# Optimization experiments

Measured on AMD Instinct MI355X. Metric: run time of the kernel, lower is better.

Reference implementation:

```python
import jax, jax.numpy as jnp
import numpy as np

T, V, E, K, D, H, BERT = 4, 4096, 4096, 32, 8, 16, 768
CAT = H + BERT  # 784, second LSTM input size


def setup_inputs() -> dict:
    key = jax.random.key(0)
    ks = jax.random.split(key, 24)
    n = lambda k, s: jax.random.normal(k, s, dtype=jnp.float32) * 0.02
    return dict(
        prices=jax.random.normal(ks[0], (T, V, 1), dtype=jnp.float32),
        node_embs=jax.random.normal(ks[1], (T, E, BERT), dtype=jnp.float32),
        he_members=jax.random.randint(ks[2], (T, E, K), 0, V),
        vert_edges=jax.random.randint(ks[3], (T, V, D), 0, E),
        Wih_p=n(ks[4], (4 * H, 1)), Whh_p=n(ks[5], (4 * H, H)),
        bih_p=n(ks[6], (4 * H,)), bhh_p=n(ks[7], (4 * H,)),
        Wih_m=n(ks[8], (4 * H, CAT)), Whh_m=n(ks[9], (4 * H, H)),
        bih_m=n(ks[10], (4 * H,)), bhh_m=n(ks[11], (4 * H,)),
        vc_trans_w=n(ks[12], (K, K, H)), vc_trans_b=n(ks[13], (K, K)),
        vc_conv_w=n(ks[14], (K,)), vc_conv_b=n(ks[15], (1,)),
        ec_w1=n(ks[16], (CAT // 4, CAT)), ec_b1=n(ks[17], (CAT // 4,)),
        ec_w2=n(ks[18], (1, CAT // 4)), ec_b2=n(ks[19], (1,)),
        attn_in=n(ks[20], (H, H)), attn_out=n(ks[21], (H, 2 * H)),
        fc_w=n(ks[22], (2, H)), fc_b=n(ks[23], (2,)),
    )


def _lstm(x, Wih, Whh, bih, bhh):
    # x: (T, B, in) -> hidden states (T, B, H); PyTorch gate order i,f,g,o
    h0 = jnp.zeros((x.shape[1], Whh.shape[1]), x.dtype)
    b = bih + bhh

    def step(carry, xt):
        h, c = carry
        g = xt @ Wih.T + h @ Whh.T + b
        i, f, gg, o = jnp.split(g, 4, axis=-1)
        c = jax.nn.sigmoid(f) * c + jax.nn.sigmoid(i) * jnp.tanh(gg)
        h = jax.nn.sigmoid(o) * jnp.tanh(c)
        return (h, c), h

    _, hs = jax.lax.scan(step, (h0, h0), x)
    return hs


def reference(prices, node_embs, he_members, vert_edges,
              Wih_p, Whh_p, bih_p, bhh_p,
              Wih_m, Whh_m, bih_m, bhh_m,
              vc_trans_w, vc_trans_b, vc_conv_w, vc_conv_b,
              ec_w1, ec_b1, ec_w2, ec_b2,
              attn_in, attn_out, fc_w, fc_b):
    # price LSTM over lookback window: (T, V, 1) -> (T, V, H)
    new_prices = _lstm(prices, Wih_p, Whh_p, bih_p, bhh_p)

    # --- VertexConv (DHGNN): gather member price embeddings per hyperedge ---
    # reg[t,e,k] = new_prices[t, he_members[t,e,k]]  -> (T, E, K, H)
    reg = jax.vmap(lambda p, idx: p[idx])(new_prices, he_members)
    # grouped Conv1d(k, k*k, dim_in, groups=k): row i of multiplier depends on feat i
    mult = jnp.einsum('tekd,kjd->tekj', reg, vc_trans_w) + vc_trans_b
    mult = jax.nn.softmax(mult, axis=-1)                     # (T,E,K,K)
    trans = jnp.einsum('tekj,tejd->tekd', mult, reg)         # (T,E,K,H)
    he_emb = jnp.einsum('tekd,k->ted', trans, vc_conv_w) + vc_conv_b  # (T,E,H)

    # concat hyperedge emb with article embedding -> (T, E, 784)
    he_cat = jnp.concatenate([he_emb, node_embs], axis=-1)

    # --- EdgeConv: per-vertex attention over its D adjacent hyperedges ---
    ft = jax.vmap(lambda h, idx: h[idx])(he_cat, vert_edges)  # (T,V,D,CAT)
    s = jax.nn.relu(ft @ ec_w1.T + ec_b1) @ ec_w2.T + ec_b2   # (T,V,D,1)
    w = jax.nn.softmax(s, axis=2)
    hg = jnp.sum(w * ft, axis=2)                              # (T,V,CAT) == scatter into hg_tensor

    # second LSTM + residual with price embeddings
    lstm_out = _lstm(hg, Wih_m, Whh_m, bih_m, bhh_m)          # (T,V,H)
    la = lstm_out + new_prices

    # torchnlp 'general' Attention: query = last step, context = all steps
    q = la[-1] @ attn_in.T                                    # (V,H)
    ctx = jnp.transpose(la, (1, 0, 2))                        # (V,T,H)
    aw = jax.nn.softmax(jnp.einsum('vd,vtd->vt', q, ctx), axis=-1)
    mix = jnp.einsum('vt,vtd->vd', aw, ctx)
    attn = jnp.tanh(jnp.concatenate([mix, q], axis=-1) @ attn_out.T)  # (V,H)

    # final classifier (dropout identity in eval)
    return attn @ fc_w.T + fc_b                               # (V,2)
```

## Files before the change

### kernel.cpp

```cpp
#include <hip/hip_runtime.h>
#include <hip/hip_bf16.h>
#include <math.h>

#define TT 4
#define VV 4096
#define EE 4096
#define KK 32
#define DD 8
#define HH 16
#define BERTD 768
#define CATD 784
#define NH 196
#define NTOT 260
#define KPB 800
#define NPB 288
#define LDB 808

typedef __bf16 bf16x8 __attribute__((ext_vector_type(8)));
typedef float  f32x4  __attribute__((ext_vector_type(4)));

__device__ __forceinline__ float sigmoidf_(float x){ return 1.0f/(1.0f+expf(-x)); }
__device__ __forceinline__ unsigned short f2bf(float f){
  __bf16 h = (__bf16)f;
  return __builtin_bit_cast(unsigned short, h);
}
__device__ __forceinline__ float bf2f(unsigned short u){
  unsigned int x = ((unsigned int)u) << 16;
  return __builtin_bit_cast(float, x);
}
__device__ __forceinline__ bf16x8 cvt_bf8(float4 a, float4 b){
  bf16x8 r;
  r[0]=(__bf16)a.x; r[1]=(__bf16)a.y; r[2]=(__bf16)a.z; r[3]=(__bf16)a.w;
  r[4]=(__bf16)b.x; r[5]=(__bf16)b.y; r[6]=(__bf16)b.z; r[7]=(__bf16)b.w;
  return r;
}

__global__ __launch_bounds__(256) void kP(
    const float* __restrict__ prices,
    const float* __restrict__ Wih, const float* __restrict__ Whh,
    const float* __restrict__ bih, const float* __restrict__ bhh,
    float* __restrict__ np_out,
    const float* __restrict__ w1, const float* __restrict__ wm,
    unsigned short* __restrict__ Bbf,
    const float* __restrict__ tw, unsigned short* __restrict__ twbf,
    float* __restrict__ esc){
  int b = blockIdx.x;
  int tid = threadIdx.x;
  if (b < 256){
    int lane = tid & 15;
    int v    = (b*256 + tid) >> 4;
    float W[4][16], wih[4], bb[4];
#pragma unroll
    for (int gi=0; gi<4; ++gi){
      int j = gi*16 + lane;
      const float4* wr = reinterpret_cast<const float4*>(&Whh[j*16]);
      float4 w0=wr[0], w1v=wr[1], w2v=wr[2], w3v=wr[3];
      W[gi][0]=w0.x; W[gi][1]=w0.y; W[gi][2]=w0.z; W[gi][3]=w0.w;
      W[gi][4]=w1v.x; W[gi][5]=w1v.y; W[gi][6]=w1v.z; W[gi][7]=w1v.w;
      W[gi][8]=w2v.x; W[gi][9]=w2v.y; W[gi][10]=w2v.z; W[gi][11]=w2v.w;
      W[gi][12]=w3v.x; W[gi][13]=w3v.y; W[gi][14]=w3v.z; W[gi][15]=w3v.w;
      wih[gi] = Wih[j];
      bb[gi]  = bih[j] + bhh[j];
    }
    float h = 0.f, c = 0.f;
    for (int t=0; t<TT; ++t){
      float x = prices[t*VV + v];
      float a0 = fmaf(x, wih[0], bb[0]);
      float a1 = fmaf(x, wih[1], bb[1]);
      float a2 = fmaf(x, wih[2], bb[2]);
      float a3 = fmaf(x, wih[3], bb[3]);
#pragma unroll
      for (int d=0; d<16; ++d){
        float hb = __shfl(h, d, 16);
        a0 = fmaf(hb, W[0][d], a0);
        a1 = fmaf(hb, W[1][d], a1);
        a2 = fmaf(hb, W[2][d], a2);
        a3 = fmaf(hb, W[3][d], a3);
      }
      float ig = sigmoidf_(a0);
      float fg = sigmoidf_(a1);
      float gg = tanhf(a2);
      float og = sigmoidf_(a3);
      c = fmaf(fg, c, ig*gg);
      h = og * tanhf(c);
      np_out[(size_t)(t*VV+v)*16 + lane] = h;
    }
  } else if (b < 544){
    int n = b - 256;
    const float* src = nullptr;
    if (n < NH)        src = &w1[(size_t)n*CATD];
    else if (n < NTOT) src = &wm[(size_t)(n-NH)*CATD];
    for (int kx = tid; kx < KPB; kx += 256){
      float v = (src != nullptr && kx < CATD) ? src[kx] : 0.f;
      Bbf[(size_t)n*KPB + kx] = f2bf(v);
    }
  } else if (b < 546){
    int base = (b - 544) * 512;
#pragma unroll
    for (int rr = 0; rr < 2; ++rr){
      int r = base + tid*2 + rr;
      const float* s = &tw[(size_t)r*16];
#pragma unroll
      for (int d = 0; d < 16; ++d) twbf[(size_t)r*16 + d] = f2bf(s[d]);
    }
  } else {
    int idx = ((b - 546)*256 + tid)*4;
    float4 z = make_float4(0.f,0.f,0.f,0.f);
    *reinterpret_cast<float4*>(&esc[idx]) = z;
  }
}

__global__ __launch_bounds__(256) void k2_fused(
    const float* __restrict__ np, const int* __restrict__ mem,
    const unsigned short* __restrict__ twbf, const float* __restrict__ tb,
    const float* __restrict__ cw, const float* __restrict__ cb,
    float* __restrict__ he_emb){
  __shared__ unsigned short s_reg[32*16*16];
  __shared__ float s_wsumP[4][16][32];
  __shared__ int   s_mem[512];
  int tid = threadIdx.x;
  int te0 = blockIdx.x * 16;
  for (int i = tid; i < 512; i += 256) s_mem[i] = mem[(size_t)te0*32 + i];
  __syncthreads();
  for (int p = tid; p < 512; p += 256){
    int gte = p & 15, gk = p >> 4;
    int t   = (te0 + gte) >> 12;
    int vid = s_mem[gte*32 + gk];
    const float4* src = reinterpret_cast<const float4*>(&np[((size_t)(t*VV) + vid)*16]);
    float4 f0 = src[0], f1 = src[1], f2 = src[2], f3 = src[3];
    uint4 u0, u1;
    u0.x = (unsigned)f2bf(f0.x) | ((unsigned)f2bf(f0.y) << 16);
    u0.y = (unsigned)f2bf(f0.z) | ((unsigned)f2bf(f0.w) << 16);
    u0.z = (unsigned)f2bf(f1.x) | ((unsigned)f2bf(f1.y) << 16);
    u0.w = (unsigned)f2bf(f1.z) | ((unsigned)f2bf(f1.w) << 16);
    u1.x = (unsigned)f2bf(f2.x) | ((unsigned)f2bf(f2.y) << 16);
    u1.y = (unsigned)f2bf(f2.z) | ((unsigned)f2bf(f2.w) << 16);
    u1.z = (unsigned)f2bf(f3.x) | ((unsigned)f2bf(f3.y) << 16);
    u1.w = (unsigned)f2bf(f3.z) | ((unsigned)f2bf(f3.w) << 16);
    uint4* dst = reinterpret_cast<uint4*>(&s_reg[(gk*16 + gte)*16]);
    dst[0] = u0; dst[1] = u1;
  }
  __syncthreads();
  int l = tid & 63;
  int w = tid >> 6;
  int lj = l & 15;
  int lg = l >> 4;
  float w0acc[4] = {0.f,0.f,0.f,0.f};
  float w1acc[4] = {0.f,0.f,0.f,0.f};
#pragma unroll
  for (int kk = 0; kk < 8; ++kk){
    int k = w*8 + kk;
    bf16x8 af = 0, b0 = 0, b1v = 0;
    if (l < 32){
      af  = *reinterpret_cast<const bf16x8*>(&s_reg[(k*16 + lj)*16 + lg*8]);
      b0  = *reinterpret_cast<const bf16x8*>(&twbf[((size_t)k*32 + lj)*16 + lg*8]);
      b1v = *reinterpret_cast<const bf16x8*>(&twbf[((size_t)k*32 + 16 + lj)*16 + lg*8]);
    }
    float tb0 = tb[k*32 + lj];
    float tb1 = tb[k*32 + 16 + lj];
    f32x4 c0 = {tb0, tb0, tb0, tb0};
    f32x4 c1 = {tb1, tb1, tb1, tb1};
    f32x4 s0 = __builtin_amdgcn_mfma_f32_16x16x32_bf16(af, b0,  c0, 0, 0, 0);
    f32x4 s1 = __builtin_amdgcn_mfma_f32_16x16x32_bf16(af, b1v, c1, 0, 0, 0);
    float cwk = cw[k];
#pragma unroll
    for (int i = 0; i < 4; ++i){
      float v0 = s0[i], v1 = s1[i];
      float m = fmaxf(v0, v1);
#pragma unroll
      for (int off = 1; off < 16; off <<= 1) m = fmaxf(m, __shfl_xor(m, off, 16));
      float e0 = expf(v0 - m), e1 = expf(v1 - m);
      float sm = e0 + e1;
#pragma unroll
      for (int off = 1; off < 16; off <<= 1) sm += __shfl_xor(sm, off, 16);
      float f = cwk / sm;
      w0acc[i] = fmaf(e0, f, w0acc[i]);
      w1acc[i] = fmaf(e1, f, w1acc[i]);
    }
  }
#pragma unroll
  for (int i = 0; i < 4; ++i){
    int ter = lg*4 + i;
    s_wsumP[w][ter][lj]      = w0acc[i];
    s_wsumP[w][ter][16 + lj] = w1acc[i];
  }
  __syncthreads();
  int te = tid >> 4, d = tid & 15;
  float he = cb[0];
#pragma unroll
  for (int j = 0; j < 32; ++j){
    float ws = s_wsumP[0][te][j] + s_wsumP[1][te][j]
             + s_wsumP[2][te][j] + s_wsumP[3][te][j];
    he = fmaf(ws, bf2f(s_reg[(j*16 + te)*16 + d]), he);
  }
  he_emb[((size_t)(te0 + te))*16 + d] = he;
}

__global__ __launch_bounds__(256) void k3_gemm_mfma(
    const float* __restrict__ he_emb, const float* __restrict__ node,
    const unsigned short* __restrict__ Bbf, const float* __restrict__ b1,
    const float* __restrict__ w2, float* __restrict__ esc,
    float* __restrict__ C_pe){
  __shared__ unsigned short Bs[48*LDB];
  int tid = threadIdx.x;
  int nc = blockIdx.x;
  int mb = blockIdx.y;
  for (int i = tid; i < 4800; i += 256){
    int r = i / 100, c = i - r*100;
    *reinterpret_cast<uint4*>(&Bs[r*LDB + c*8]) =
      *reinterpret_cast<const uint4*>(&Bbf[(size_t)(nc*48 + r)*KPB + c*8]);
  }
  __syncthreads();
  int l = tid & 63, w = tid >> 6;
  int lr = l & 15, ls = l >> 4;
  int m0 = mb*128 + w*32;
  int row0 = m0 + lr, row1 = m0 + 16 + lr;
  const unsigned short* bbase = &Bs[lr*LDB + ls*8];
  f32x4 acc[2][3] = {};
#pragma unroll
  for (int s = 0; s < 25; ++s){
    bf16x8 af0 = 0, af1 = 0;
    if (s == 0){
      if (ls < 2){
        const float4* p0 = reinterpret_cast<const float4*>(&he_emb[(size_t)row0*16 + ls*8]);
        const float4* p1 = reinterpret_cast<const float4*>(&he_emb[(size_t)row1*16 + ls*8]);
        af0 = cvt_bf8(p0[0], p0[1]);
        af1 = cvt_bf8(p1[0], p1[1]);
      } else {
        const float4* p0 = reinterpret_cast<const float4*>(&node[(size_t)row0*BERTD + ls*8 - 16]);
        const float4* p1 = reinterpret_cast<const float4*>(&node[(size_t)row1*BERTD + ls*8 - 16]);
        af0 = cvt_bf8(p0[0], p0[1]);
        af1 = cvt_bf8(p1[0], p1[1]);
      }
    } else if (!(s == 24 && ls >= 2)){
      int ko = s*32 + ls*8 - 16;
      const float4* p0 = reinterpret_cast<const float4*>(&node[(size_t)row0*BERTD + ko]);
      const float4* p1 = reinterpret_cast<const float4*>(&node[(size_t)row1*BERTD + ko]);
      af0 = cvt_bf8(p0[0], p0[1]);
      af1 = cvt_bf8(p1[0], p1[1]);
    }
#pragma unroll
    for (int j = 0; j < 3; ++j){
      bf16x8 bfv = *reinterpret_cast<const bf16x8*>(&bbase[j*16*LDB + s*32]);
      acc[0][j] = __builtin_amdgcn_mfma_f32_16x16x32_bf16(af0, bfv, acc[0][j], 0, 0, 0);
      acc[1][j] = __builtin_amdgcn_mfma_f32_16x16x32_bf16(af1, bfv, acc[1][j], 0, 0, 0);
    }
  }
  float p[2][4] = {{0.f,0.f,0.f,0.f},{0.f,0.f,0.f,0.f}};
#pragma unroll
  for (int j = 0; j < 3; ++j){
    int n = nc*48 + j*16 + lr;
    bool hid = (n < NH);
    float b1n = hid ? b1[n] : 0.f;
    float w2n = hid ? w2[n] : 0.f;
#pragma unroll
    for (int i = 0; i < 2; ++i){
#pragma unroll
      for (int q = 0; q < 4; ++q){
        float v = acc[i][j][q];
        if (hid){
          p[i][q] += fmaxf(v + b1n, 0.f) * w2n;
        } else if (n < NTOT){
          int m = m0 + i*16 + ls*4 + q;
          C_pe[(size_t)m*64 + (n - NH)] = v;
        }
      }
    }
  }
  if (nc*48 < NH){
#pragma unroll
    for (int i = 0; i < 2; ++i){
#pragma unroll
      for (int q = 0; q < 4; ++q){
        float v = p[i][q];
#pragma unroll
        for (int off = 1; off < 16; off <<= 1) v += __shfl_xor(v, off, 16);
        if (lr == 0){
          int m = m0 + i*16 + ls*4 + q;
          atomicAdd(&esc[m], v);
        }
      }
    }
  }
}

__global__ __launch_bounds__(256) void k456(
    const int* __restrict__ ve, const float* __restrict__ esc,
    const float* __restrict__ C_pe, const float* __restrict__ np,
    const float* __restrict__ Whh, const float* __restrict__ bih,
    const float* __restrict__ bhh,
    const float* __restrict__ ain, const float* __restrict__ aout,
    const float* __restrict__ fcw, const float* __restrict__ fcb,
    float* __restrict__ out){
  __shared__ float s_ain[16*17];
  __shared__ float s_aout[16*33];
  __shared__ float s_fc[32];
  __shared__ float s_fcb[2];
  int tid = threadIdx.x;
  { int j = tid >> 4, d = tid & 15; s_ain[j*17+d] = ain[tid]; }
  for (int i = tid; i < 512; i += 256){ int j = i >> 5, d = i & 31; s_aout[j*33+d] = aout[i]; }
  if (tid < 32) s_fc[tid] = fcw[tid];
  if (tid < 2)  s_fcb[tid] = fcb[tid];
  int lane = tid & 15;
  int v = (blockIdx.x*256 + tid) >> 4;
  float W[4][16], b[4];
#pragma unroll
  for (int gi=0; gi<4; ++gi){
    int j = gi*16 + lane;
    const float4* wr = reinterpret_cast<const float4*>(&Whh[j*16]);
    float4 w0=wr[0], w1=wr[1], w2=wr[2], w3=wr[3];
    W[gi][0]=w0.x; W[gi][1]=w0.y; W[gi][2]=w0.z; W[gi][3]=w0.w;
    W[gi][4]=w1.x; W[gi][5]=w1.y; W[gi][6]=w1.z; W[gi][7]=w1.w;
    W[gi][8]=w2.x; W[gi][9]=w2.y; W[gi][10]=w2.z; W[gi][11]=w2.w;
    W[gi][12]=w3.x; W[gi][13]=w3.y; W[gi][14]=w3.z; W[gi][15]=w3.w;
    b[gi] = bih[j] + bhh[j];
  }
  __syncthreads();
  float h = 0.f, c = 0.f;
  float la0, la1, la2, la3;
#pragma unroll
  for (int t=0; t<TT; ++t){
    const int* vp = &ve[((size_t)(t*VV) + v)*8];
    int e[8]; float wv[8];
    float mx = -1e30f;
#pragma unroll
    for (int d = 0; d < 8; ++d){
      e[d] = vp[d];
      wv[d] = esc[(t << 12) + e[d]];
      mx = fmaxf(mx, wv[d]);
    }
    float s = 0.f;
#pragma unroll
    for (int d = 0; d < 8; ++d){ wv[d] = expf(wv[d]-mx); s += wv[d]; }
    float inv = 1.f/s;
#pragma unroll
    for (int d = 0; d < 8; ++d) wv[d] *= inv;
    float g0 = b[0], g1 = b[1], g2 = b[2], g3 = b[3];
#pragma unroll
    for (int d = 0; d < 8; ++d){
      const float* cp = &C_pe[(size_t)((t << 12) + e[d])*64];
      g0 = fmaf(wv[d], cp[lane],      g0);
      g1 = fmaf(wv[d], cp[16 + lane], g1);
      g2 = fmaf(wv[d], cp[32 + lane], g2);
      g3 = fmaf(wv[d], cp[48 + lane], g3);
    }
#pragma unroll
    for (int d=0; d<16; ++d){
      float hb = __shfl(h, d, 16);
      g0 = fmaf(hb, W[0][d], g0);
      g1 = fmaf(hb, W[1][d], g1);
      g2 = fmaf(hb, W[2][d], g2);
      g3 = fmaf(hb, W[3][d], g3);
    }
    float ig = sigmoidf_(g0);
    float fg = sigmoidf_(g1);
    float gg = tanhf(g2);
    float og = sigmoidf_(g3);
    c = fmaf(fg, c, ig*gg);
    h = og * tanhf(c);
    float la = h + np[(size_t)(t*VV+v)*16 + lane];
    if (t == 0) la0 = la; else if (t == 1) la1 = la;
    else if (t == 2) la2 = la; else la3 = la;
  }
  float q = 0.f;
#pragma unroll
  for (int d=0; d<16; ++d){
    float bb = __shfl(la3, d, 16);
    q = fmaf(bb, s_ain[lane*17+d], q);
  }
  float aw0 = q*la0, aw1 = q*la1, aw2 = q*la2, aw3 = q*la3;
#pragma unroll
  for (int off=1; off<16; off<<=1){
    aw0 += __shfl_xor(aw0, off, 16);
    aw1 += __shfl_xor(aw1, off, 16);
    aw2 += __shfl_xor(aw2, off, 16);
    aw3 += __shfl_xor(aw3, off, 16);
  }
  float mx = fmaxf(fmaxf(aw0,aw1), fmaxf(aw2,aw3));
  aw0 = expf(aw0-mx); aw1 = expf(aw1-mx); aw2 = expf(aw2-mx); aw3 = expf(aw3-mx);
  float inv = 1.f/(aw0+aw1+aw2+aw3);
  float mix = (aw0*la0 + aw1*la1 + aw2*la2 + aw3*la3) * inv;
  float a = 0.f;
#pragma unroll
  for (int d=0; d<16; ++d){
    float m  = __shfl(mix, d, 16);
    float qq = __shfl(q,  d, 16);
    a = fmaf(m,  s_aout[lane*33+d],    a);
    a = fmaf(qq, s_aout[lane*33+16+d], a);
  }
  float at = tanhf(a);
  float p0 = at * s_fc[lane];
  float p1 = at * s_fc[16+lane];
#pragma unroll
  for (int off=1; off<16; off<<=1){
    p0 += __shfl_xor(p0, off, 16);
    p1 += __shfl_xor(p1, off, 16);
  }
  if (lane == 0){
    out[(size_t)v*2 + 0] = p0 + s_fcb[0];
    out[(size_t)v*2 + 1] = p1 + s_fcb[1];
  }
}

extern "C" void kernel_launch(void* const* d_in, const int* in_sizes, int n_in,
                              void* d_out, int out_size, void* d_ws, size_t ws_size,
                              hipStream_t stream){
  const float* prices = (const float*)d_in[0];
  const float* node   = (const float*)d_in[1];
  const int*   mem    = (const int*)d_in[2];
  const int*   ve     = (const int*)d_in[3];
  const float* Wih_p  = (const float*)d_in[4];
  const float* Whh_p  = (const float*)d_in[5];
  const float* bih_p  = (const float*)d_in[6];
  const float* bhh_p  = (const float*)d_in[7];
  const float* Wih_m  = (const float*)d_in[8];
  const float* Whh_m  = (const float*)d_in[9];
  const float* bih_m  = (const float*)d_in[10];
  const float* bhh_m  = (const float*)d_in[11];
  const float* tw     = (const float*)d_in[12];
  const float* tb     = (const float*)d_in[13];
  const float* cw     = (const float*)d_in[14];
  const float* cb     = (const float*)d_in[15];
  const float* w1     = (const float*)d_in[16];
  const float* b1     = (const float*)d_in[17];
  const float* w2     = (const float*)d_in[18];
  const float* ain    = (const float*)d_in[20];
  const float* aout   = (const float*)d_in[21];
  const float* fcw    = (const float*)d_in[22];
  const float* fcb    = (const float*)d_in[23];

  float* np_buf = (float*)d_ws;
  float* he_emb = np_buf + (size_t)TT*VV*HH;
  float* esc    = he_emb + (size_t)TT*EE*HH;
  float* C_pe   = esc    + (size_t)TT*EE;
  unsigned short* Bbf  = (unsigned short*)(C_pe + (size_t)TT*EE*64);
  unsigned short* twbf = Bbf + (size_t)NPB*KPB;

  kP<<<562, 256, 0, stream>>>(prices, Wih_p, Whh_p, bih_p, bhh_p, np_buf,
                              w1, Wih_m, Bbf, tw, twbf, esc);
  k2_fused<<<(TT*EE)/16, 256, 0, stream>>>(np_buf, mem, twbf, tb, cw, cb, he_emb);
  k3_gemm_mfma<<<dim3(6, 128), 256, 0, stream>>>(he_emb, node, Bbf, b1, w2, esc, C_pe);
  k456<<<(VV*16)/256, 256, 0, stream>>>(ve, esc, C_pe, np_buf, Whh_m, bih_m, bhh_m,
                                        ain, aout, fcw, fcb, (float*)d_out);
}
```

Before: 232.7 us.

## Pre-convert node embeddings to a padded bf16 A matrix and regroup GEMM blocks

Adds extra kP blocks that convert node_embs to bf16 in a padded row-major A buffer, and k2 now writes he_emb as bf16 straight into the first 16 columns of that buffer. The GEMM then loads A tiles with plain 16-byte bf16 loads instead of fp32 loads with per-element conversion and branching. It also linearises the GEMM grid so that six N-chunks of eight M-blocks are scheduled together, which should improve L2 reuse of A rows. The cost is an extra full pass that reads the fp32 embeddings and writes a bf16 copy before the GEMM.

```diff
diff --git a/kernel.cpp b/kernel.cpp
--- a/kernel.cpp
+++ b/kernel.cpp
@@ -28,11 +28,13 @@
   unsigned int x = ((unsigned int)u) << 16;
   return __builtin_bit_cast(float, x);
 }
-__device__ __forceinline__ bf16x8 cvt_bf8(float4 a, float4 b){
-  bf16x8 r;
-  r[0]=(__bf16)a.x; r[1]=(__bf16)a.y; r[2]=(__bf16)a.z; r[3]=(__bf16)a.w;
-  r[4]=(__bf16)b.x; r[5]=(__bf16)b.y; r[6]=(__bf16)b.z; r[7]=(__bf16)b.w;
-  return r;
+__device__ __forceinline__ uint4 pack8(float4 a, float4 b){
+  uint4 u;
+  u.x = (unsigned)f2bf(a.x) | ((unsigned)f2bf(a.y) << 16);
+  u.y = (unsigned)f2bf(a.z) | ((unsigned)f2bf(a.w) << 16);
+  u.z = (unsigned)f2bf(b.x) | ((unsigned)f2bf(b.y) << 16);
+  u.w = (unsigned)f2bf(b.z) | ((unsigned)f2bf(b.w) << 16);
+  return u;
 }
 
 __global__ __launch_bounds__(256) void kP(
@@ -43,7 +45,8 @@
     const float* __restrict__ w1, const float* __restrict__ wm,
     unsigned short* __restrict__ Bbf,
     const float* __restrict__ tw, unsigned short* __restrict__ twbf,
-    float* __restrict__ esc){
+    float* __restrict__ esc,
+    const float* __restrict__ node, unsigned short* __restrict__ Abf){
   int b = blockIdx.x;
   int tid = threadIdx.x;
   if (b < 256){
@@ -103,10 +106,27 @@
 #pragma unroll
       for (int d = 0; d < 16; ++d) twbf[(size_t)r*16 + d] = f2bf(s[d]);
     }
-  } else {
+  } else if (b < 562){
     int idx = ((b - 546)*256 + tid)*4;
     float4 z = make_float4(0.f,0.f,0.f,0.f);
     *reinterpret_cast<float4*>(&esc[idx]) = z;
+  } else {
+    int row = (b - 562)*16 + (tid >> 4);
+    int c0  = (tid & 15) * 48;
+    const float* src = &node[(size_t)row*BERTD + c0];
+    unsigned short* dst = &Abf[(size_t)row*KPB + 16 + c0];
+#pragma unroll
+    for (int cc = 0; cc < 6; ++cc){
+      float4 f0 = *reinterpret_cast<const float4*>(&src[cc*8]);
+      float4 f1 = *reinterpret_cast<const float4*>(&src[cc*8+4]);
+      *reinterpret_cast<uint4*>(&dst[cc*8]) = pack8(f0, f1);
+    }
+    if ((tid & 15) == 15){
+      uint4 z = {0,0,0,0};
+      unsigned short* zp = &Abf[(size_t)row*KPB + 784];
+      *reinterpret_cast<uint4*>(&zp[0]) = z;
+      *reinterpret_cast<uint4*>(&zp[8]) = z;
+    }
   }
 }
 
@@ -114,7 +134,7 @@
     const float* __restrict__ np, const int* __restrict__ mem,
     const unsigned short* __restrict__ twbf, const float* __restrict__ tb,
     const float* __restrict__ cw, const float* __restrict__ cb,
-    float* __restrict__ he_emb){
+    unsigned short* __restrict__ Abf){
   __shared__ unsigned short s_reg[32*16*16];
   __shared__ float s_wsumP[4][16][32];
   __shared__ int   s_mem[512];
@@ -128,17 +148,9 @@
     int vid = s_mem[gte*32 + gk];
     const float4* src = reinterpret_cast<const float4*>(&np[((size_t)(t*VV) + vid)*16]);
     float4 f0 = src[0], f1 = src[1], f2 = src[2], f3 = src[3];
-    uint4 u0, u1;
-    u0.x = (unsigned)f2bf(f0.x) | ((unsigned)f2bf(f0.y) << 16);
-    u0.y = (unsigned)f2bf(f0.z) | ((unsigned)f2bf(f0.w) << 16);
-    u0.z = (unsigned)f2bf(f1.x) | ((unsigned)f2bf(f1.y) << 16);
-    u0.w = (unsigned)f2bf(f1.z) | ((unsigned)f2bf(f1.w) << 16);
-    u1.x = (unsigned)f2bf(f2.x) | ((unsigned)f2bf(f2.y) << 16);
-    u1.y = (unsigned)f2bf(f2.z) | ((unsigned)f2bf(f2.w) << 16);
-    u1.z = (unsigned)f2bf(f3.x) | ((unsigned)f2bf(f3.y) << 16);
-    u1.w = (unsigned)f2bf(f3.z) | ((unsigned)f2bf(f3.w) << 16);
     uint4* dst = reinterpret_cast<uint4*>(&s_reg[(gk*16 + gte)*16]);
-    dst[0] = u0; dst[1] = u1;
+    dst[0] = pack8(f0, f1);
+    dst[1] = pack8(f2, f3);
   }
   __syncthreads();
   int l = tid & 63;
@@ -193,18 +205,22 @@
              + s_wsumP[2][te][j] + s_wsumP[3][te][j];
     he = fmaf(ws, bf2f(s_reg[(j*16 + te)*16 + d]), he);
   }
-  he_emb[((size_t)(te0 + te))*16 + d] = he;
+  Abf[((size_t)(te0 + te))*KPB + d] = f2bf(he);
 }
 
 __global__ __launch_bounds__(256) void k3_gemm_mfma(
-    const float* __restrict__ he_emb, const float* __restrict__ node,
+    const unsigned short* __restrict__ Abf,
     const unsigned short* __restrict__ Bbf, const float* __restrict__ b1,
     const float* __restrict__ w2, float* __restrict__ esc,
     float* __restrict__ C_pe){
   __shared__ unsigned short Bs[48*LDB];
   int tid = threadIdx.x;
-  int nc = blockIdx.x;
-  int mb = blockIdx.y;
+  int bid = blockIdx.x;
+  int group = bid / 48;
+  int within = bid - group*48;
+  int nc  = within >> 3;
+  int mbr = within & 7;
+  int mb  = group*8 + mbr;
   for (int i = tid; i < 4800; i += 256){
     int r = i / 100, c = i - r*100;
     *reinterpret_cast<uint4*>(&Bs[r*LDB + c*8]) =
@@ -214,31 +230,14 @@
   int l = tid & 63, w = tid >> 6;
   int lr = l & 15, ls = l >> 4;
   int m0 = mb*128 + w*32;
-  int row0 = m0 + lr, row1 = m0 + 16 + lr;
+  const unsigned short* a0p = &Abf[(size_t)(m0 + lr)*KPB];
+  const unsigned short* a1p = a0p + (size_t)16*KPB;
   const unsigned short* bbase = &Bs[lr*LDB + ls*8];
   f32x4 acc[2][3] = {};
 #pragma unroll
   for (int s = 0; s < 25; ++s){
-    bf16x8 af0 = 0, af1 = 0;
-    if (s == 0){
-      if (ls < 2){
-        const float4* p0 = reinterpret_cast<const float4*>(&he_emb[(size_t)row0*16 + ls*8]);
-        const float4* p1 = reinterpret_cast<const float4*>(&he_emb[(size_t)row1*16 + ls*8]);
-        af0 = cvt_bf8(p0[0], p0[1]);
-        af1 = cvt_bf8(p1[0], p1[1]);
-      } else {
-        const float4* p0 = reinterpret_cast<const float4*>(&node[(size_t)row0*BERTD + ls*8 - 16]);
-        const float4* p1 = reinterpret_cast<const float4*>(&node[(size_t)row1*BERTD + ls*8 - 16]);
-        af0 = cvt_bf8(p0[0], p0[1]);
-        af1 = cvt_bf8(p1[0], p1[1]);
-      }
-    } else if (!(s == 24 && ls >= 2)){
-      int ko = s*32 + ls*8 - 16;
-      const float4* p0 = reinterpret_cast<const float4*>(&node[(size_t)row0*BERTD + ko]);
-      const float4* p1 = reinterpret_cast<const float4*>(&node[(size_t)row1*BERTD + ko]);
-      af0 = cvt_bf8(p0[0], p0[1]);
-      af1 = cvt_bf8(p1[0], p1[1]);
-    }
+    bf16x8 af0 = *reinterpret_cast<const bf16x8*>(&a0p[s*32 + ls*8]);
+    bf16x8 af1 = *reinterpret_cast<const bf16x8*>(&a1p[s*32 + ls*8]);
 #pragma unroll
     for (int j = 0; j < 3; ++j){
       bf16x8 bfv = *reinterpret_cast<const bf16x8*>(&bbase[j*16*LDB + s*32]);
@@ -430,16 +429,16 @@
   const float* fcb    = (const float*)d_in[23];
 
   float* np_buf = (float*)d_ws;
-  float* he_emb = np_buf + (size_t)TT*VV*HH;
-  float* esc    = he_emb + (size_t)TT*EE*HH;
+  float* esc    = np_buf + (size_t)TT*VV*HH;
   float* C_pe   = esc    + (size_t)TT*EE;
   unsigned short* Bbf  = (unsigned short*)(C_pe + (size_t)TT*EE*64);
   unsigned short* twbf = Bbf + (size_t)NPB*KPB;
-
-  kP<<<562, 256, 0, stream>>>(prices, Wih_p, Whh_p, bih_p, bhh_p, np_buf,
-                              w1, Wih_m, Bbf, tw, twbf, esc);
-  k2_fused<<<(TT*EE)/16, 256, 0, stream>>>(np_buf, mem, twbf, tb, cw, cb, he_emb);
-  k3_gemm_mfma<<<dim3(6, 128), 256, 0, stream>>>(he_emb, node, Bbf, b1, w2, esc, C_pe);
+  unsigned short* Abf  = twbf + (size_t)1024*16;
+
+  kP<<<1586, 256, 0, stream>>>(prices, Wih_p, Whh_p, bih_p, bhh_p, np_buf,
+                               w1, Wih_m, Bbf, tw, twbf, esc, node, Abf);
+  k2_fused<<<(TT*EE)/16, 256, 0, stream>>>(np_buf, mem, twbf, tb, cw, cb, Abf);
+  k3_gemm_mfma<<<768, 256, 0, stream>>>(Abf, Bbf, b1, w2, esc, C_pe);
   k456<<<(VV*16)/256, 256, 0, stream>>>(ve, esc, C_pe, np_buf, Whh_m, bih_m, bhh_m,
                                         ain, aout, fcw, fcb, (float*)d_out);
 }
```

New measurement: 211.9 us. -8.9%, faster.
